# Performance work log

Measured on AMD Instinct MI355X. Metric: run time of the kernel, lower is better.

## Reference

```python
import jax, jax.numpy as jnp
import numpy as np
from jax import lax

B, T, C_IN = 64, 1000, 12
D_MODEL, D_STATE, D_CONV, EXPAND = 128, 16, 4, 2
D_INNER = EXPAND * D_MODEL          # 256
DT_RANK = (D_MODEL + 15) // 16      # ceil(d_model/16) = 8
NUM_CLASSES = 5


def setup_inputs() -> dict:
    key = jax.random.key(0)
    ks = jax.random.split(key, 12)
    s = 0.05
    f = jnp.float32
    return {
        "x": jax.random.normal(ks[0], (B, T, C_IN), f),
        # input projection Linear(C_IN, D_MODEL) with bias
        "ip_w": jax.random.normal(ks[1], (D_MODEL, C_IN), f) * s,
        "ip_b": jnp.zeros((D_MODEL,), f),
        # Mamba block params (mamba_ssm layout)
        "in_proj_w": jax.random.normal(ks[2], (2 * D_INNER, D_MODEL), f) * s,
        "conv_w": jax.random.normal(ks[3], (D_INNER, D_CONV), f) * s,
        "conv_b": jnp.zeros((D_INNER,), f),
        "x_proj_w": jax.random.normal(ks[4], (DT_RANK + 2 * D_STATE, D_INNER), f) * s,
        "dt_proj_w": jax.random.normal(ks[5], (D_INNER, DT_RANK), f) * s,
        "dt_proj_b": jax.random.uniform(ks[6], (D_INNER,), f, -4.0, -2.0),  # softplus -> small positive dt
        "A_log": jnp.log(jnp.tile(jnp.arange(1, D_STATE + 1, dtype=f), (D_INNER, 1))),
        "D_skip": jnp.ones((D_INNER,), f),
        "out_proj_w": jax.random.normal(ks[7], (D_MODEL, D_INNER), f) * s,
        # classifier head: Linear(128,64) -> ReLU -> Linear(64,5)
        "fc1_w": jax.random.normal(ks[8], (64, D_MODEL), f) * s,
        "fc1_b": jnp.zeros((64,), f),
        "fc2_w": jax.random.normal(ks[9], (NUM_CLASSES, 64), f) * s,
        "fc2_b": jnp.zeros((NUM_CLASSES,), f),
    }


def _silu(x):
    return x * jax.nn.sigmoid(x)


def _mamba(h, in_proj_w, conv_w, conv_b, x_proj_w, dt_proj_w, dt_proj_b,
           A_log, D_skip, out_proj_w):
    # h: (B, T, D_MODEL)
    xz = h @ in_proj_w.T                              # (B, T, 2*Di)
    xm, z = jnp.split(xz, 2, axis=-1)
    # depthwise causal conv over time (pad left d_conv-1)
    xp = jnp.pad(xm, ((0, 0), (D_CONV - 1, 0), (0, 0)))
    rhs = conv_w.T[:, None, :]                        # (d_conv, 1, Di)
    xc = lax.conv_general_dilated(
        xp, rhs, (1,), 'VALID',
        dimension_numbers=('NHC', 'HIO', 'NHC'),
        feature_group_count=D_INNER) + conv_b
    u = _silu(xc)                                     # (B, T, Di)
    dbc = u @ x_proj_w.T                              # (B, T, dt_rank + 2N)
    dt = dbc[..., :DT_RANK]
    Bm = dbc[..., DT_RANK:DT_RANK + D_STATE]          # (B, T, N)
    Cm = dbc[..., DT_RANK + D_STATE:]                 # (B, T, N)
    delta = jax.nn.softplus(dt @ dt_proj_w.T + dt_proj_b)  # (B, T, Di)
    A = -jnp.exp(A_log)                               # (Di, N)

    def step(hst, inp):
        d_t, b_t, c_t, u_t = inp                      # (B,Di),(B,N),(B,N),(B,Di)
        dA = jnp.exp(d_t[..., None] * A)              # (B, Di, N)
        hst = dA * hst + (d_t * u_t)[..., None] * b_t[:, None, :]
        y_t = jnp.einsum('bdn,bn->bd', hst, c_t)
        return hst, y_t

    h0 = jnp.zeros((h.shape[0], D_INNER, D_STATE), h.dtype)
    _, ys = lax.scan(step, h0, (delta.transpose(1, 0, 2), Bm.transpose(1, 0, 2),
                                Cm.transpose(1, 0, 2), u.transpose(1, 0, 2)))
    y = ys.transpose(1, 0, 2) + u * D_skip            # (B, T, Di)
    y = y * _silu(z)
    return y @ out_proj_w.T                           # (B, T, D_MODEL)


def reference(x, ip_w, ip_b, in_proj_w, conv_w, conv_b, x_proj_w, dt_proj_w,
              dt_proj_b, A_log, D_skip, out_proj_w, fc1_w, fc1_b, fc2_w, fc2_b):
    h = x @ ip_w.T + ip_b                             # (B, T, D_MODEL)
    y = _mamba(h, in_proj_w, conv_w, conv_b, x_proj_w, dt_proj_w, dt_proj_b,
               A_log, D_skip, out_proj_w)
    last = y[:, -1, :]                                # (B, D_MODEL)
    hid = jax.nn.relu(last @ fc1_w.T + fc1_b)
    return hid @ fc2_w.T + fc2_b                      # (B, NUM_CLASSES)
```

## Files before the change

kernel.cpp:

```cpp
#include <hip/hip_runtime.h>
#include <cstddef>

#define T_LEN 1000
#define B_SZ 64
#define C_IN_ 12
#define D_MODEL_ 128
#define D_INNER_ 256
#define D_STATE_ 16
#define DT_RANK_ 8
#define N_CLS 5

typedef __attribute__((ext_vector_type(8))) short bf16x8;
typedef __attribute__((ext_vector_type(8))) unsigned short u16x8;
typedef __attribute__((ext_vector_type(4))) float f32x4;

__device__ __forceinline__ float fast_exp2(float x) {
#if __has_builtin(__builtin_amdgcn_exp2f)
  return __builtin_amdgcn_exp2f(x);
#else
  float r; asm volatile("v_exp_f32 %0, %1" : "=v"(r) : "v"(x)); return r;
#endif
}
__device__ __forceinline__ float fast_log2(float x) {
#if __has_builtin(__builtin_amdgcn_logf)
  return __builtin_amdgcn_logf(x);
#else
  float r; asm volatile("v_log_f32 %0, %1" : "=v"(r) : "v"(x)); return r;
#endif
}
__device__ __forceinline__ float fast_rcp(float x) {
#if __has_builtin(__builtin_amdgcn_rcpf)
  return __builtin_amdgcn_rcpf(x);
#else
  float r; asm volatile("v_rcp_f32 %0, %1" : "=v"(r) : "v"(x)); return r;
#endif
}
__device__ __forceinline__ float silu_f(float x) {
  float den = 1.f + fast_exp2(-x * 1.4426950408889634f);
  return x * fast_rcp(den);
}
__device__ __forceinline__ float softplus_f(float x) {
  const float L = 1.4426950408889634f, iL = 0.6931471805599453f;
  float e = fast_exp2(-fabsf(x) * L);
  float l = fast_log2(1.f + e) * iL;
  return fmaxf(x, 0.f) + l;
}
__device__ __forceinline__ unsigned short f2bf(float f) {
  unsigned u = __builtin_bit_cast(unsigned, f);
  u = u + 0x7FFFu + ((u >> 16) & 1u);
  return (unsigned short)(u >> 16);
}
__device__ __forceinline__ float bf2f(unsigned short h) {
  unsigned u = ((unsigned)h) << 16;
  return __builtin_bit_cast(float, u);
}

__global__ __launch_bounds__(256) void k0_prep(
    const float* __restrict__ x, const float* __restrict__ ip_w,
    const float* __restrict__ ip_b, const float* __restrict__ in_proj_w,
    char* __restrict__ h_pk, char* __restrict__ w_pk)
{
  __shared__ unsigned short pk_s[8192];
  __shared__ unsigned short pkw_s[32768];
  const int tid = threadIdx.x;

  if (blockIdx.x == 16) {
    if (blockIdx.y != 0) return;
    const int n = tid;
    for (int k = 0; k < D_MODEL_; ++k) {
      unsigned short v = f2bf(in_proj_w[(size_t)n * D_MODEL_ + k]);
      int off = ((n >> 4) * 4 + (k >> 5)) * 512 + ((k & 31) >> 3) * 128
              + (n & 15) * 8 + (k & 7);
      pkw_s[off] = v;
    }
    __syncthreads();
    const float4* s4 = (const float4*)pkw_s;
    float4* dst = (float4*)w_pk;
#pragma unroll
    for (int q = 0; q < 16; ++q) dst[tid * 16 + q] = s4[tid * 16 + q];
    return;
  }

  const int tile4 = blockIdx.x;
  const int b = blockIdx.y;
  const int rl = tid & 63;
  const int kc = (tid >> 6) * 32;
  const int t = tile4 * 64 + rl;

  float xr[C_IN_] = {0.f, 0.f, 0.f, 0.f, 0.f, 0.f, 0.f, 0.f, 0.f, 0.f, 0.f, 0.f};
  const bool valid = (t < T_LEN);
  if (valid) {
    const float4* xp = (const float4*)(x + ((size_t)b * T_LEN + t) * C_IN_);
    float4 v0 = xp[0], v1 = xp[1], v2 = xp[2];
    xr[0] = v0.x; xr[1] = v0.y; xr[2] = v0.z;  xr[3] = v0.w;
    xr[4] = v1.x; xr[5] = v1.y; xr[6] = v1.z;  xr[7] = v1.w;
    xr[8] = v2.x; xr[9] = v2.y; xr[10] = v2.z; xr[11] = v2.w;
  }
  for (int kk = 0; kk < 32; ++kk) {
    const int k = kc + kk;
    unsigned short v = 0;
    if (valid) {
      float acc = ip_b[k];
      const float* wr = ip_w + k * C_IN_;
#pragma unroll
      for (int c = 0; c < C_IN_; ++c) acc += xr[c] * wr[c];
      v = f2bf(acc);
    }
    int off = (rl >> 4) * 2048 + (k >> 5) * 512 + ((k & 31) >> 3) * 128
            + (rl & 15) * 8 + (k & 7);
    pk_s[off] = v;
  }
  __syncthreads();
  const float4* s4 = (const float4*)pk_s;
  float4* dst = (float4*)(h_pk + (size_t)(b * 64 + tile4 * 4) * 4096);
#pragma unroll
  for (int q = 0; q < 4; ++q) dst[tid * 4 + q] = s4[tid * 4 + q];
}

__global__ __launch_bounds__(256) void k1_u(
    const char* __restrict__ h_pk, const char* __restrict__ w_pk,
    const float* __restrict__ conv_w, const float* __restrict__ conv_b,
    float* __restrict__ u_out)
{
  __shared__ float xm[67][260];

  const int tile = blockIdx.x;
  const int b    = blockIdx.y;
  const int t0   = tile * 64;
  const int tid  = threadIdx.x;
  const int w    = tid >> 6;
  const int l    = tid & 63;

  {
    const char* achunk = h_pk + (size_t)(b * 64 + tile * 4 + w) * 4096;
    bf16x8 a0 = *(const bf16x8*)(achunk + 0 * 1024 + l * 16);
    bf16x8 a1 = *(const bf16x8*)(achunk + 1 * 1024 + l * 16);
    bf16x8 a2 = *(const bf16x8*)(achunk + 2 * 1024 + l * 16);
    bf16x8 a3 = *(const bf16x8*)(achunk + 3 * 1024 + l * 16);

    const int row_l = w * 16 + (l >> 4) * 4;
#pragma unroll
    for (int nt = 0; nt < 16; ++nt) {
      const char* wb = w_pk + (size_t)nt * 4096 + l * 16;
      bf16x8 b0 = *(const bf16x8*)(wb + 0 * 1024);
      bf16x8 b1 = *(const bf16x8*)(wb + 1 * 1024);
      bf16x8 b2 = *(const bf16x8*)(wb + 2 * 1024);
      bf16x8 b3 = *(const bf16x8*)(wb + 3 * 1024);
      f32x4 acc = {0.f, 0.f, 0.f, 0.f};
      acc = __builtin_amdgcn_mfma_f32_16x16x32_bf16(a0, b0, acc, 0, 0, 0);
      acc = __builtin_amdgcn_mfma_f32_16x16x32_bf16(a1, b1, acc, 0, 0, 0);
      acc = __builtin_amdgcn_mfma_f32_16x16x32_bf16(a2, b2, acc, 0, 0, 0);
      acc = __builtin_amdgcn_mfma_f32_16x16x32_bf16(a3, b3, acc, 0, 0, 0);
      const int col = nt * 16 + (l & 15);
#pragma unroll
      for (int r = 0; r < 4; ++r)
        xm[3 + row_l + r][col] = acc[r];
    }
  }

  {
    const int n = tid;
    float hac[3] = {0.f, 0.f, 0.f};
    if (tile > 0) {
      const char* wrow = w_pk + (size_t)(n >> 4) * 4096 + (n & 15) * 16;
#pragma unroll
      for (int kt = 0; kt < 4; ++kt)
#pragma unroll
        for (int lg = 0; lg < 4; ++lg) {
          u16x8 wv = *(const u16x8*)(wrow + kt * 1024 + lg * 256);
#pragma unroll
          for (int r = 0; r < 3; ++r) {
            const int t = t0 - 3 + r;
            const char* hc = h_pk + (size_t)(b * 64 + (t >> 4)) * 4096;
            u16x8 hv = *(const u16x8*)(hc + kt * 1024 + lg * 256 + (t & 15) * 16);
#pragma unroll
            for (int j = 0; j < 8; ++j) hac[r] += bf2f(hv[j]) * bf2f(wv[j]);
          }
        }
    }
#pragma unroll
    for (int r = 0; r < 3; ++r) xm[r][n] = hac[r];
  }
  __syncthreads();

  {
    const int n = tid;
    const float4 cw = *(const float4*)&conv_w[n * 4];
    const float  cb = conv_b[n];
    float x0 = xm[0][n], x1 = xm[1][n], x2 = xm[2][n];
    for (int i = 0; i < 64; ++i) {
      const int t = t0 + i;
      float x3 = xm[3 + i][n];
      if (t < T_LEN) {
        float s = cb + x0 * cw.x + x1 * cw.y + x2 * cw.z + x3 * cw.w;
        u_out[(((size_t)b * T_LEN + t) << 8) + n] = silu_f(s);
      }
      x0 = x1; x1 = x2; x2 = x3;
    }
  }
}

__global__ __launch_bounds__(256) void k3_delta(
    const float* __restrict__ u, const float* __restrict__ x_proj_w,
    const float* __restrict__ dt_proj_w, const float* __restrict__ dt_proj_b,
    float* __restrict__ pk_delta, float* __restrict__ pk_du,
    float* __restrict__ pk_bm)
{
  __shared__ float4 xp4[24][65];
  __shared__ float dt_s[64][9];
  __shared__ float bm_s[64][17];

  const int row0 = blockIdx.x * 64;
  const int tid = threadIdx.x;

  for (int f = tid; f < 24 * 64; f += 256) {
    int c = f >> 6, k4 = f & 63;
    xp4[c][k4] = *(const float4*)&x_proj_w[(size_t)c * 256 + k4 * 4];
  }
  const float4 w0 = *(const float4*)&dt_proj_w[(size_t)tid * 8];
  const float4 w1 = *(const float4*)&dt_proj_w[(size_t)tid * 8 + 4];
  const float bias = dt_proj_b[tid];
  __syncthreads();

  {
    const int r2 = tid >> 3, cg = tid & 7;
    const int ra = 2 * r2;
    const float4* ua4 = (const float4*)(u + (size_t)(row0 + ra) * 256);
    const float4* ub4 = (const float4*)(u + (size_t)(row0 + ra + 1) * 256);
    float a0 = 0.f, a1 = 0.f, a2 = 0.f, b0 = 0.f, b1 = 0.f, b2 = 0.f;
    for (int k4 = 0; k4 < 64; ++k4) {
      float4 a = ua4[k4], bb = ub4[k4];
      float4 q0 = xp4[cg * 3 + 0][k4];
      float4 q1 = xp4[cg * 3 + 1][k4];
      float4 q2 = xp4[cg * 3 + 2][k4];
      a0 += a.x * q0.x + a.y * q0.y + a.z * q0.z + a.w * q0.w;
      a1 += a.x * q1.x + a.y * q1.y + a.z * q1.z + a.w * q1.w;
      a2 += a.x * q2.x + a.y * q2.y + a.z * q2.z + a.w * q2.w;
      b0 += bb.x * q0.x + bb.y * q0.y + bb.z * q0.z + bb.w * q0.w;
      b1 += bb.x * q1.x + bb.y * q1.y + bb.z * q1.z + bb.w * q1.w;
      b2 += bb.x * q2.x + bb.y * q2.y + bb.z * q2.z + bb.w * q2.w;
    }
    float va[2][3] = {{a0, a1, a2}, {b0, b1, b2}};
#pragma unroll
    for (int rr = 0; rr < 2; ++rr)
#pragma unroll
      for (int c = 0; c < 3; ++c) {
        int col = cg * 3 + c;
        int row = ra + rr;
        if (col < 8) dt_s[row][col] = va[rr][c];
        else bm_s[row][col - 8] = va[rr][c];
      }
  }
  __syncthreads();

  for (int g = 0; g < 8; ++g) {
    float dd[8], uu[8];
#pragma unroll
    for (int j = 0; j < 8; ++j) {
      int r = g * 8 + j;
      float pre = bias
        + dt_s[r][0] * w0.x + dt_s[r][1] * w0.y + dt_s[r][2] * w0.z + dt_s[r][3] * w0.w
        + dt_s[r][4] * w1.x + dt_s[r][5] * w1.y + dt_s[r][6] * w1.z + dt_s[r][7] * w1.w;
      float dlt = softplus_f(pre);
      size_t o = (size_t)(row0 + r) * 256 + tid;
      dd[j] = dlt;
      uu[j] = dlt * u[o];
    }
    int row = row0 + g * 8;
    int bb_ = row / 1000;
    int t   = row - bb_ * 1000;
    size_t base = (((size_t)bb_ * 250 + (t >> 2)) * 256 + tid) * 4;
    *(float4*)&pk_delta[base]        = make_float4(dd[0], dd[1], dd[2], dd[3]);
    *(float4*)&pk_delta[base + 1024] = make_float4(dd[4], dd[5], dd[6], dd[7]);
    *(float4*)&pk_du[base]           = make_float4(uu[0], uu[1], uu[2], uu[3]);
    *(float4*)&pk_du[base + 1024]    = make_float4(uu[4], uu[5], uu[6], uu[7]);
  }
  if (tid < 16) {
    for (int g = 0; g < 8; ++g) {
      float pb[8];
#pragma unroll
      for (int j = 0; j < 8; ++j) pb[j] = bm_s[g * 8 + j][tid];
      int row = row0 + g * 8;
      int bb_ = row / 1000;
      int t   = row - bb_ * 1000;
      size_t base = (((size_t)bb_ * 250 + (t >> 2)) * 16 + tid) * 4;
      *(float4*)&pk_bm[base]      = make_float4(pb[0], pb[1], pb[2], pb[3]);
      *(float4*)&pk_bm[base + 64] = make_float4(pb[4], pb[5], pb[6], pb[7]);
    }
  }
}

__global__ __launch_bounds__(256) void k4_scan(
    const float* __restrict__ pk_delta, const float* __restrict__ pk_du,
    const float* __restrict__ pk_bm, const float* __restrict__ A_log,
    float* __restrict__ state_out)
{
  const int d0 = blockIdx.x * 16;
  const int b  = blockIdx.y;
  const int tid = threadIdx.x;
  const int dl = tid >> 4;
  const int n  = tid & 15;
  const int d  = d0 + dl;

  const float A2 = -expf(A_log[(size_t)d * 16 + n]) * 1.4426950408889634f;
  float s = 0.f;

  const float* dp = pk_delta + ((size_t)b * 250 * 256 + d) * 4;
  const float* xp = pk_du    + ((size_t)b * 250 * 256 + d) * 4;
  const float* bp = pk_bm    + ((size_t)b * 250 * 16 + n) * 4;

#pragma unroll 2
  for (int t4 = 0; t4 < 250; ++t4) {
    float4 dv = *(const float4*)(dp + (size_t)t4 * 1024);
    float4 xv = *(const float4*)(xp + (size_t)t4 * 1024);
    float4 bv = *(const float4*)(bp + (size_t)t4 * 64);
    s = fast_exp2(dv.x * A2) * s + xv.x * bv.x;
    s = fast_exp2(dv.y * A2) * s + xv.y * bv.y;
    s = fast_exp2(dv.z * A2) * s + xv.z * bv.z;
    s = fast_exp2(dv.w * A2) * s + xv.w * bv.w;
  }
  state_out[((size_t)b * 256 + d) * 16 + n] = s;
}

__global__ __launch_bounds__(256) void k5_head(
    const float* __restrict__ x, const float* __restrict__ ip_w,
    const float* __restrict__ ip_b, const float* __restrict__ in_proj_w,
    const float* __restrict__ x_proj_w, const float* __restrict__ u,
    const float* __restrict__ state, const float* __restrict__ D_skip,
    const float* __restrict__ out_proj_w, const float* __restrict__ fc1_w,
    const float* __restrict__ fc1_b, const float* __restrict__ fc2_w,
    const float* __restrict__ fc2_b, float* __restrict__ out)
{
  const int b = blockIdx.x, tid = threadIdx.x;
  __shared__ float hl[128], ul[256], zs[256], cm[16], yv[256], ov[128], hid[64];
  if (tid < 128) {
    float acc = ip_b[tid];
    const float* xr = x + ((size_t)b * T_LEN + (T_LEN - 1)) * C_IN_;
#pragma unroll
    for (int c = 0; c < C_IN_; ++c) acc += xr[c] * ip_w[tid * C_IN_ + c];
    hl[tid] = acc;
  }
  ul[tid] = u[((size_t)b * T_LEN + (T_LEN - 1)) * 256 + tid];
  __syncthreads();
  {
    float acc = 0.f;
    const float4* wv = (const float4*)(in_proj_w + (size_t)(256 + tid) * 128);
    const float4* h4 = (const float4*)hl;
    for (int k = 0; k < 32; ++k) {
      float4 a = wv[k], c = h4[k];
      acc += c.x * a.x + c.y * a.y + c.z * a.z + c.w * a.w;
    }
    zs[tid] = silu_f(acc);
  }
  if (tid < 16) {
    float acc = 0.f;
    const float4* wv = (const float4*)(x_proj_w + (size_t)(24 + tid) * 256);
    const float4* u4 = (const float4*)ul;
    for (int k = 0; k < 64; ++k) {
      float4 a = wv[k], c = u4[k];
      acc += c.x * a.x + c.y * a.y + c.z * a.z + c.w * a.w;
    }
    cm[tid] = acc;
  }
  __syncthreads();
  {
    const float* st = state + ((size_t)b * 256 + tid) * 16;
    float acc = 0.f;
#pragma unroll
    for (int n = 0; n < 16; ++n) acc += st[n] * cm[n];
    yv[tid] = (acc + ul[tid] * D_skip[tid]) * zs[tid];
  }
  __syncthreads();
  if (tid < 128) {
    float acc = 0.f;
    const float4* wv = (const float4*)(out_proj_w + (size_t)tid * 256);
    const float4* y4 = (const float4*)yv;
    for (int k = 0; k < 64; ++k) {
      float4 a = wv[k], c = y4[k];
      acc += c.x * a.x + c.y * a.y + c.z * a.z + c.w * a.w;
    }
    ov[tid] = acc;
  }
  __syncthreads();
  if (tid < 64) {
    float acc = fc1_b[tid];
    const float4* wv = (const float4*)(fc1_w + (size_t)tid * 128);
    const float4* o4 = (const float4*)ov;
    for (int k = 0; k < 32; ++k) {
      float4 a = wv[k], c = o4[k];
      acc += c.x * a.x + c.y * a.y + c.z * a.z + c.w * a.w;
    }
    hid[tid] = fmaxf(acc, 0.f);
  }
  __syncthreads();
  if (tid < N_CLS) {
    float acc = fc2_b[tid];
    const float* wv = fc2_w + (size_t)tid * 64;
    for (int k = 0; k < 64; ++k) acc += hid[k] * wv[k];
    out[b * N_CLS + tid] = acc;
  }
}

extern "C" void kernel_launch(void* const* d_in, const int* in_sizes, int n_in,
                              void* d_out, int out_size, void* d_ws, size_t ws_size,
                              hipStream_t stream) {
  (void)in_sizes; (void)n_in; (void)out_size; (void)ws_size;
  const float* x         = (const float*)d_in[0];
  const float* ip_w      = (const float*)d_in[1];
  const float* ip_b      = (const float*)d_in[2];
  const float* in_proj_w = (const float*)d_in[3];
  const float* conv_w    = (const float*)d_in[4];
  const float* conv_b    = (const float*)d_in[5];
  const float* x_proj_w  = (const float*)d_in[6];
  const float* dt_proj_w = (const float*)d_in[7];
  const float* dt_proj_b = (const float*)d_in[8];
  const float* A_log     = (const float*)d_in[9];
  const float* D_skip    = (const float*)d_in[10];
  const float* out_proj_w= (const float*)d_in[11];
  const float* fc1_w     = (const float*)d_in[12];
  const float* fc1_b     = (const float*)d_in[13];
  const float* fc2_w     = (const float*)d_in[14];
  const float* fc2_b     = (const float*)d_in[15];
  float* out = (float*)d_out;

  float* u     = (float*)d_ws;
  float* delta = u + (size_t)16384000;
  float* du    = delta + (size_t)16384000;
  float* bm    = du + (size_t)16384000;
  float* state = bm + (size_t)1024000;
  char* h_pk = (char*)delta;
  char* w_pk = h_pk + (size_t)64 * 64 * 4096;

  k0_prep<<<dim3(17, 64), 256, 0, stream>>>(x, ip_w, ip_b, in_proj_w, h_pk, w_pk);
  k1_u<<<dim3(16, 64), 256, 0, stream>>>(h_pk, w_pk, conv_w, conv_b, u);
  k3_delta<<<1000, 256, 0, stream>>>(u, x_proj_w, dt_proj_w, dt_proj_b, delta, du, bm);
  k4_scan<<<dim3(16, 64), 256, 0, stream>>>(delta, du, bm, A_log, state);
  k5_head<<<64, 256, 0, stream>>>(x, ip_w, ip_b, in_proj_w, x_proj_w, u, state,
                                  D_skip, out_proj_w, fc1_w, fc1_b, fc2_w, fc2_b, out);
}
```

Measured before the change: 227.4 us.

## Split selective scan into time chunks with a combine pass

The sequential scan over 1000 timesteps is cut into 5 chunks that run in parallel across a third grid dimension. Each chunk records its local end state and the product of its decays (exp of A times the summed delta), and a new combine kernel chains the chunks together. Loads are also software-prefetched one step ahead. This multiplies the number of blocks five-fold to hide the latency of the serial recurrence. The cost is an extra launch and extra exp/sum work, and the scratch buffers reuse the u region, so the last-timestep u is now saved separately in k3.

```diff
diff --git a/kernel.cpp b/kernel.cpp
--- a/kernel.cpp
+++ b/kernel.cpp
@@ -9,6 +9,8 @@
 #define D_STATE_ 16
 #define DT_RANK_ 8
 #define N_CLS 5
+#define NCH 5
+#define CT4 50
 
 typedef __attribute__((ext_vector_type(8))) short bf16x8;
 typedef __attribute__((ext_vector_type(8))) unsigned short u16x8;
@@ -204,7 +206,7 @@
     const float* __restrict__ u, const float* __restrict__ x_proj_w,
     const float* __restrict__ dt_proj_w, const float* __restrict__ dt_proj_b,
     float* __restrict__ pk_delta, float* __restrict__ pk_du,
-    float* __restrict__ pk_bm)
+    float* __restrict__ pk_bm, float* __restrict__ u_last)
 {
   __shared__ float4 xp4[24][65];
   __shared__ float dt_s[64][9];
@@ -263,8 +265,12 @@
         + dt_s[r][4] * w1.x + dt_s[r][5] * w1.y + dt_s[r][6] * w1.z + dt_s[r][7] * w1.w;
       float dlt = softplus_f(pre);
       size_t o = (size_t)(row0 + r) * 256 + tid;
+      float uv = u[o];
       dd[j] = dlt;
-      uu[j] = dlt * u[o];
+      uu[j] = dlt * uv;
+      int rowg = row0 + r;
+      if ((rowg - (rowg / 1000) * 1000) == 999)
+        u_last[(rowg / 1000) * 256 + tid] = uv;
     }
     int row = row0 + g * 8;
     int bb_ = row / 1000;
@@ -293,39 +299,64 @@
 __global__ __launch_bounds__(256) void k4_scan(
     const float* __restrict__ pk_delta, const float* __restrict__ pk_du,
     const float* __restrict__ pk_bm, const float* __restrict__ A_log,
-    float* __restrict__ state_out)
+    float* __restrict__ Qb, float* __restrict__ Pb)
 {
   const int d0 = blockIdx.x * 16;
   const int b  = blockIdx.y;
+  const int c  = blockIdx.z;
   const int tid = threadIdx.x;
   const int dl = tid >> 4;
   const int n  = tid & 15;
   const int d  = d0 + dl;
 
   const float A2 = -expf(A_log[(size_t)d * 16 + n]) * 1.4426950408889634f;
-  float s = 0.f;
-
-  const float* dp = pk_delta + ((size_t)b * 250 * 256 + d) * 4;
-  const float* xp = pk_du    + ((size_t)b * 250 * 256 + d) * 4;
-  const float* bp = pk_bm    + ((size_t)b * 250 * 16 + n) * 4;
-
-#pragma unroll 2
-  for (int t4 = 0; t4 < 250; ++t4) {
-    float4 dv = *(const float4*)(dp + (size_t)t4 * 1024);
-    float4 xv = *(const float4*)(xp + (size_t)t4 * 1024);
-    float4 bv = *(const float4*)(bp + (size_t)t4 * 64);
+  float s = 0.f, sum = 0.f;
+
+  const float* dp = pk_delta + ((size_t)b * 250 * 256 + d) * 4 + (size_t)c * CT4 * 1024;
+  const float* xp = pk_du    + ((size_t)b * 250 * 256 + d) * 4 + (size_t)c * CT4 * 1024;
+  const float* bp = pk_bm    + ((size_t)b * 250 * 16 + n) * 4 + (size_t)c * CT4 * 64;
+
+  float4 dv = *(const float4*)dp;
+  float4 xv = *(const float4*)xp;
+  float4 bv = *(const float4*)bp;
+  for (int i = 0; i < CT4 - 1; ++i) {
+    float4 dvn = *(const float4*)(dp + (size_t)(i + 1) * 1024);
+    float4 xvn = *(const float4*)(xp + (size_t)(i + 1) * 1024);
+    float4 bvn = *(const float4*)(bp + (size_t)(i + 1) * 64);
+    sum += (dv.x + dv.y) + (dv.z + dv.w);
     s = fast_exp2(dv.x * A2) * s + xv.x * bv.x;
     s = fast_exp2(dv.y * A2) * s + xv.y * bv.y;
     s = fast_exp2(dv.z * A2) * s + xv.z * bv.z;
     s = fast_exp2(dv.w * A2) * s + xv.w * bv.w;
-  }
-  state_out[((size_t)b * 256 + d) * 16 + n] = s;
+    dv = dvn; xv = xvn; bv = bvn;
+  }
+  sum += (dv.x + dv.y) + (dv.z + dv.w);
+  s = fast_exp2(dv.x * A2) * s + xv.x * bv.x;
+  s = fast_exp2(dv.y * A2) * s + xv.y * bv.y;
+  s = fast_exp2(dv.z * A2) * s + xv.z * bv.z;
+  s = fast_exp2(dv.w * A2) * s + xv.w * bv.w;
+
+  const size_t o = (size_t)c * 262144 + (size_t)b * 4096 + (size_t)d0 * 16 + tid;
+  Qb[o] = s;
+  Pb[o] = fast_exp2(A2 * sum);
+}
+
+__global__ __launch_bounds__(256) void k4b_combine(
+    const float* __restrict__ Qb, const float* __restrict__ Pb,
+    float* __restrict__ state_out)
+{
+  const size_t g = (size_t)blockIdx.x * 256 + threadIdx.x;
+  float s = Qb[g];
+#pragma unroll
+  for (int c = 1; c < NCH; ++c)
+    s = Qb[(size_t)c * 262144 + g] + Pb[(size_t)c * 262144 + g] * s;
+  state_out[g] = s;
 }
 
 __global__ __launch_bounds__(256) void k5_head(
     const float* __restrict__ x, const float* __restrict__ ip_w,
     const float* __restrict__ ip_b, const float* __restrict__ in_proj_w,
-    const float* __restrict__ x_proj_w, const float* __restrict__ u,
+    const float* __restrict__ x_proj_w, const float* __restrict__ u_last,
     const float* __restrict__ state, const float* __restrict__ D_skip,
     const float* __restrict__ out_proj_w, const float* __restrict__ fc1_w,
     const float* __restrict__ fc1_b, const float* __restrict__ fc2_w,
@@ -340,7 +371,7 @@
     for (int c = 0; c < C_IN_; ++c) acc += xr[c] * ip_w[tid * C_IN_ + c];
     hl[tid] = acc;
   }
-  ul[tid] = u[((size_t)b * T_LEN + (T_LEN - 1)) * 256 + tid];
+  ul[tid] = u_last[b * 256 + tid];
   __syncthreads();
   {
     float acc = 0.f;
@@ -423,18 +454,23 @@
   const float* fc2_b     = (const float*)d_in[15];
   float* out = (float*)d_out;
 
-  float* u     = (float*)d_ws;
-  float* delta = u + (size_t)16384000;
-  float* du    = delta + (size_t)16384000;
-  float* bm    = du + (size_t)16384000;
-  float* state = bm + (size_t)1024000;
+  float* u      = (float*)d_ws;
+  float* delta  = u + (size_t)16384000;
+  float* du     = delta + (size_t)16384000;
+  float* bm     = du + (size_t)16384000;
+  float* state  = bm + (size_t)1024000;
+  float* u_last = state + (size_t)262144;
   char* h_pk = (char*)delta;
   char* w_pk = h_pk + (size_t)64 * 64 * 4096;
+  float* Qb  = u;
+  float* Pb  = u + (size_t)2000000;
 
   k0_prep<<<dim3(17, 64), 256, 0, stream>>>(x, ip_w, ip_b, in_proj_w, h_pk, w_pk);
   k1_u<<<dim3(16, 64), 256, 0, stream>>>(h_pk, w_pk, conv_w, conv_b, u);
-  k3_delta<<<1000, 256, 0, stream>>>(u, x_proj_w, dt_proj_w, dt_proj_b, delta, du, bm);
-  k4_scan<<<dim3(16, 64), 256, 0, stream>>>(delta, du, bm, A_log, state);
-  k5_head<<<64, 256, 0, stream>>>(x, ip_w, ip_b, in_proj_w, x_proj_w, u, state,
+  k3_delta<<<1000, 256, 0, stream>>>(u, x_proj_w, dt_proj_w, dt_proj_b,
+                                     delta, du, bm, u_last);
+  k4_scan<<<dim3(16, 64, NCH), 256, 0, stream>>>(delta, du, bm, A_log, Qb, Pb);
+  k4b_combine<<<1024, 256, 0, stream>>>(Qb, Pb, state);
+  k5_head<<<64, 256, 0, stream>>>(x, ip_w, ip_b, in_proj_w, x_proj_w, u_last, state,
                                   D_skip, out_proj_w, fc1_w, fc1_b, fc2_w, fc2_b, out);
 }
```

New measurement: 219.7 us. -3.4%, faster.
